# Kernel tuning notes

Measured on AMD Instinct MI355X. Metric: run time of the kernel, lower is better.

Reference implementation:

```python
import jax, jax.numpy as jnp
import numpy as np

INF = 1.0e10
EPS = 1e-12

def setup_inputs() -> dict:
    key = jax.random.key(0)
    k1, k2 = jax.random.split(key)
    B, N, A = 512, 16384, 64
    return {
        "residue_ca_pos": jax.random.normal(k1, (B, N, 3), dtype=jnp.float32) * 10.0,
        "residue_mask": jnp.ones((B, N), dtype=jnp.float32),
        "atom_pos": jax.random.normal(k2, (B, A, 3), dtype=jnp.float32) * 10.0,
        "atom_mask": jnp.ones((B, A), dtype=jnp.float32),
        "max_p": 1,
        "top_k": 4096,
    }

def reference(residue_ca_pos, residue_mask, atom_pos, atom_mask, max_p, top_k):
    # ligand centroid per batch: [B, 3]
    centroid = atom_pos.sum(-2) / atom_mask.sum(-1, keepdims=True)
    # distance from centroid to each residue Ca, invalid residues pushed to +inf
    diff = centroid[:, None, :] - residue_ca_pos            # [B, N, 3]
    dists = jnp.sqrt(jnp.sum(diff * diff, axis=-1) + EPS) + (1.0 - residue_mask) * INF
    # k smallest distances -> neighbor indices [B, top_k]
    _, nbr_indices = jax.lax.top_k(-dists, top_k)
    rows = jnp.arange(residue_mask.shape[0])[:, None]       # [B, 1]
    # scatter writes building the masks (faithful to torch scatter_ with constants)
    residue_spatial_mask = residue_mask.at[rows, nbr_indices].set(0.0)
    residue_spatial_mask_esm = (1.0 - residue_mask).at[rows, nbr_indices].set(32.0)
    return residue_spatial_mask, residue_spatial_mask_esm
```

## Files before the change

kernel.cpp:

```cpp
#include <hip/hip_runtime.h>

#pragma clang fp contract(off)

#define B_   512
#define N_   16384
#define A_   64
#define TPB  1024
#define CAP  2048
#define ITERS 4

__global__ __launch_bounds__(TPB) void fused_kernel(
    const float* __restrict__ pos,   const float* __restrict__ mask,
    const float* __restrict__ apos,  const float* __restrict__ amask,
    const int*   __restrict__ topk_ptr,
    float* __restrict__ out0, float* __restrict__ out1)
{
#pragma clang fp contract(off)
    __shared__ unsigned short dist16[N_];
    __shared__ unsigned       hist[2048];
    __shared__ unsigned       hist2[32];
    __shared__ unsigned       cand_bits[CAP];
    __shared__ unsigned short cand_idx[CAP];
    __shared__ float          s_atoms[A_ * 3 + A_];
    __shared__ float          s_c[3];
    __shared__ unsigned       s_B11, s_less11, s_P16, s_j, s_ncand, s_k;

    const int tid = threadIdx.x;
    const int b   = blockIdx.x;
    const float* __restrict__ p = pos  + (size_t)b * N_ * 3;
    const float* __restrict__ m = mask + (size_t)b * N_;

    hist[tid]        = 0u;
    hist[tid + 1024] = 0u;
    if (tid < 32) hist2[tid] = 0u;
    if (tid < 256)
        s_atoms[tid] = (tid < 192) ? apos[(size_t)b * 192 + tid]
                                   : amask[(size_t)b * 64 + (tid - 192)];
    if (tid == 0) {
        s_ncand = 0u;
        int kk = *topk_ptr;
        if (kk < 0)  kk = 0;
        if (kk > N_) kk = N_;
        s_k = (unsigned)kk;
    }
    __syncthreads();

    if (tid < 64) {
        float comp = 0.0f, ms = 0.0f;
        if (tid < 3) {
            comp = s_atoms[tid];
            for (int a = 1; a < A_; ++a) comp += s_atoms[a * 3 + tid];
        }
        if (tid == 3) {
            const float* am = s_atoms + 192;
            float r0 = am[0], r1 = am[1], r2 = am[2], r3 = am[3];
            float r4 = am[4], r5 = am[5], r6 = am[6], r7 = am[7];
            for (int i = 8; i < A_; i += 8) {
                r0 += am[i + 0]; r1 += am[i + 1]; r2 += am[i + 2]; r3 += am[i + 3];
                r4 += am[i + 4]; r5 += am[i + 5]; r6 += am[i + 6]; r7 += am[i + 7];
            }
            ms = ((r0 + r1) + (r2 + r3)) + ((r4 + r5) + (r6 + r7));
        }
        ms = __shfl(ms, 3, 64);
        if (tid < 3) s_c[tid] = comp / ms;
    }
    __syncthreads();

    const float cx = s_c[0], cy = s_c[1], cz = s_c[2];
    const unsigned k = s_k;

    unsigned rbits[ITERS * 4];
    float    rm[ITERS * 4];
#pragma unroll
    for (int it = 0; it < ITERS; ++it) {
        const int i0 = it * (TPB * 4) + tid * 4;
        const float4 pa = *(const float4*)(p + (size_t)i0 * 3);
        const float4 pb = *(const float4*)(p + (size_t)i0 * 3 + 4);
        const float4 pc = *(const float4*)(p + (size_t)i0 * 3 + 8);
        const float4 mv = *(const float4*)(m + i0);
        const float px[4] = {pa.x, pa.w, pb.z, pc.y};
        const float py[4] = {pa.y, pb.x, pb.w, pc.z};
        const float pz[4] = {pa.z, pb.y, pc.x, pc.w};
        const float mm[4] = {mv.x, mv.y, mv.z, mv.w};
        unsigned short loc[4];
#pragma unroll
        for (int j = 0; j < 4; ++j) {
            float dx = cx - px[j], dy = cy - py[j], dz = cz - pz[j];
            float dx2 = dx * dx, dy2 = dy * dy, dz2 = dz * dz;
            float s = (dx2 + dy2) + dz2;
            s = s + 1e-12f;
            float d = sqrtf(s);
            float im = (1.0f - mm[j]) * 1e10f;
            d = d + im;
            const unsigned bits = __float_as_uint(d);
            rbits[it * 4 + j] = bits;
            rm[it * 4 + j]    = mm[j];
            loc[j] = (unsigned short)(bits >> 16);
            atomicAdd(&hist[bits >> 21], 1u);
        }
        *(ushort4*)&dist16[i0] = make_ushort4(loc[0], loc[1], loc[2], loc[3]);
    }
    __syncthreads();

    if (k > 0) {
        if (tid < 64) {
            unsigned s = 0;
#pragma unroll
            for (int i = 0; i < 32; ++i) s += hist[tid * 32 + i];
            unsigned incl = s;
#pragma unroll
            for (int off = 1; off < 64; off <<= 1) {
                unsigned v = (unsigned)__shfl_up((int)incl, off, 64);
                if (tid >= off) incl += v;
            }
            unsigned long long bal = __ballot(incl >= k);
            const int g = __ffsll(bal) - 1;
            const unsigned cum1 = (unsigned)__shfl((int)(incl - s), g, 64);

            unsigned h2 = (tid < 32) ? hist[g * 32 + tid] : 0u;
            unsigned incl2 = h2;
#pragma unroll
            for (int off = 1; off < 64; off <<= 1) {
                unsigned v = (unsigned)__shfl_up((int)incl2, off, 64);
                if (tid >= off) incl2 += v;
            }
            unsigned long long bal2 = __ballot(tid < 32 && (cum1 + incl2 >= k));
            const int sb = __ffsll(bal2) - 1;
            const unsigned cum2 = cum1 + (unsigned)__shfl((int)(incl2 - h2), sb, 64);
            if (tid == 0) { s_B11 = (unsigned)(g * 32 + sb); s_less11 = cum2; }
        }
        __syncthreads();
        const unsigned B11 = s_B11;

#pragma unroll
        for (int x = 0; x < ITERS * 4; ++x) {
            const unsigned v = rbits[x] >> 16;
            if ((v >> 5) == B11) atomicAdd(&hist2[v & 31u], 1u);
        }
        __syncthreads();
        if (tid < 64) {
            unsigned h = (tid < 32) ? hist2[tid] : 0u;
            unsigned incl = h;
#pragma unroll
            for (int off = 1; off < 64; off <<= 1) {
                unsigned v = (unsigned)__shfl_up((int)incl, off, 64);
                if (tid >= off) incl += v;
            }
            const unsigned less11 = s_less11;
            unsigned long long bal = __ballot(tid < 32 && (less11 + incl >= k));
            const int sb = __ffsll(bal) - 1;
            const unsigned cumx = less11 + (unsigned)__shfl((int)(incl - h), sb, 64);
            if (tid == 0) { s_P16 = (B11 << 5) | (unsigned)sb; s_j = k - cumx; }
        }
        __syncthreads();
        const unsigned P16 = s_P16;
        const unsigned j   = s_j;

#pragma unroll
        for (int it = 0; it < ITERS; ++it) {
#pragma unroll
            for (int jj = 0; jj < 4; ++jj) {
                const unsigned bits = rbits[it * 4 + jj];
                if ((bits >> 16) == P16) {
                    const unsigned w = atomicAdd(&s_ncand, 1u);
                    if (w < CAP) {
                        cand_bits[w] = bits;
                        cand_idx[w]  = (unsigned short)(it * (TPB * 4) + tid * 4 + jj);
                    }
                }
            }
        }
        __syncthreads();

        const unsigned c = min(s_ncand, (unsigned)CAP);
        for (unsigned t = tid; t < c; t += TPB) {
            const unsigned bt = cand_bits[t];
            const unsigned it = cand_idx[t];
            unsigned rank = 0;
            for (unsigned u = 0; u < c; ++u) {
                const unsigned bu = cand_bits[u];
                rank += (bu < bt) || (bu == bt && (unsigned)cand_idx[u] < it);
            }
            if (rank < j) dist16[it] = 0;
        }
        __syncthreads();
    }

    const unsigned P16f = (k > 0) ? s_P16 : 0u;
#pragma unroll
    for (int it = 0; it < ITERS; ++it) {
        const int i0 = it * (TPB * 4) + tid * 4;
        const ushort4 dv = *(const ushort4*)&dist16[i0];
        const unsigned short dvs[4] = {dv.x, dv.y, dv.z, dv.w};
        float4 o0, o1;
        float* o0p = &o0.x; float* o1p = &o1.x;
#pragma unroll
        for (int jj = 0; jj < 4; ++jj) {
            const bool sel = (unsigned)dvs[jj] < P16f;
            const float mv = rm[it * 4 + jj];
            o0p[jj] = sel ? 0.0f  : mv;
            o1p[jj] = sel ? 32.0f : (1.0f - mv);
        }
        *(float4*)(out0 + (size_t)b * N_ + i0) = o0;
        *(float4*)(out1 + (size_t)b * N_ + i0) = o1;
    }
}

extern "C" void kernel_launch(void* const* d_in, const int* in_sizes, int n_in,
                              void* d_out, int out_size, void* d_ws, size_t ws_size,
                              hipStream_t stream) {
    const float* pos   = (const float*)d_in[0];
    const float* rmask = (const float*)d_in[1];
    const float* apos  = (const float*)d_in[2];
    const float* amask = (const float*)d_in[3];
    const int*   topk  = (const int*)d_in[5];

    float* out0 = (float*)d_out;
    float* out1 = out0 + (size_t)B_ * N_;

    fused_kernel<<<B_, TPB, 0, stream>>>(pos, rmask, apos, amask, topk, out0, out1);
}
```

Before: 210.2 us.

## Stream inputs via triple-buffered global_load_lds pipeline and drop LDS distance array

Replaces direct per-thread float4 global loads with a 3-deep ring of asynchronous global-to-LDS copies (global_load_lds) overlapped with distance computation, using explicit vmcnt waits and barriers per chunk. Removes the 16-bit distance array in LDS by encoding candidate slots into the register-held bits and storing selection flags per candidate. Output writes become scalar per-thread coalesced stores instead of float4. The change lowers LDS footprint for occupancy and overlaps load latency, but adds two barriers per chunk and narrower stores.

```diff
diff --git a/kernel.cpp b/kernel.cpp
--- a/kernel.cpp
+++ b/kernel.cpp
@@ -2,28 +2,38 @@
 
 #pragma clang fp contract(off)
 
-#define B_   512
-#define N_   16384
-#define A_   64
-#define TPB  1024
-#define CAP  2048
-#define ITERS 4
-
-__global__ __launch_bounds__(TPB) void fused_kernel(
+#define B_     512
+#define N_     16384
+#define A_     64
+#define TPB    1024
+#define CAP    2048
+#define NCHUNK 16
+#define NBUF   3
+
+#define AS1 __attribute__((address_space(1)))
+#define AS3 __attribute__((address_space(3)))
+
+__device__ __forceinline__ void gl2lds16(const float* g, float* l) {
+    __builtin_amdgcn_global_load_lds((const AS1 unsigned int*)g,
+                                     (AS3 unsigned int*)l, 16, 0, 0);
+}
+
+__global__ __launch_bounds__(TPB, 8) void fused_kernel(
     const float* __restrict__ pos,   const float* __restrict__ mask,
     const float* __restrict__ apos,  const float* __restrict__ amask,
     const int*   __restrict__ topk_ptr,
     float* __restrict__ out0, float* __restrict__ out1)
 {
 #pragma clang fp contract(off)
-    __shared__ unsigned short dist16[N_];
+    __shared__ __align__(16) float stage[NBUF][4096];
     __shared__ unsigned       hist[2048];
     __shared__ unsigned       hist2[32];
     __shared__ unsigned       cand_bits[CAP];
     __shared__ unsigned short cand_idx[CAP];
+    __shared__ unsigned char  sel_flags[CAP];
     __shared__ float          s_atoms[A_ * 3 + A_];
     __shared__ float          s_c[3];
-    __shared__ unsigned       s_B11, s_less11, s_P16, s_j, s_ncand, s_k;
+    __shared__ unsigned s_B11, s_less11, s_P16, s_j, s_ncand, s_k;
 
     const int tid = threadIdx.x;
     const int b   = blockIdx.x;
@@ -43,6 +53,15 @@
         if (kk > N_) kk = N_;
         s_k = (unsigned)kk;
     }
+
+    {
+        const float* g0 = (tid < 768) ? (p + tid * 4)            : (m + (tid - 768) * 4);
+        const float* g1 = (tid < 768) ? (p + 3072 + tid * 4)     : (m + 1024 + (tid - 768) * 4);
+        const float* g2 = (tid < 768) ? (p + 2 * 3072 + tid * 4) : (m + 2 * 1024 + (tid - 768) * 4);
+        gl2lds16(g0, &stage[0][tid * 4]);
+        gl2lds16(g1, &stage[1][tid * 4]);
+        gl2lds16(g2, &stage[2][tid * 4]);
+    }
     __syncthreads();
 
     if (tid < 64) {
@@ -69,36 +88,43 @@
     const float cx = s_c[0], cy = s_c[1], cz = s_c[2];
     const unsigned k = s_k;
 
-    unsigned rbits[ITERS * 4];
-    float    rm[ITERS * 4];
-#pragma unroll
-    for (int it = 0; it < ITERS; ++it) {
-        const int i0 = it * (TPB * 4) + tid * 4;
-        const float4 pa = *(const float4*)(p + (size_t)i0 * 3);
-        const float4 pb = *(const float4*)(p + (size_t)i0 * 3 + 4);
-        const float4 pc = *(const float4*)(p + (size_t)i0 * 3 + 8);
-        const float4 mv = *(const float4*)(m + i0);
-        const float px[4] = {pa.x, pa.w, pb.z, pc.y};
-        const float py[4] = {pa.y, pb.x, pb.w, pc.z};
-        const float pz[4] = {pa.z, pb.y, pc.x, pc.w};
-        const float mm[4] = {mv.x, mv.y, mv.z, mv.w};
-        unsigned short loc[4];
-#pragma unroll
-        for (int j = 0; j < 4; ++j) {
-            float dx = cx - px[j], dy = cy - py[j], dz = cz - pz[j];
-            float dx2 = dx * dx, dy2 = dy * dy, dz2 = dz * dz;
-            float s = (dx2 + dy2) + dz2;
-            s = s + 1e-12f;
-            float d = sqrtf(s);
-            float im = (1.0f - mm[j]) * 1e10f;
-            d = d + im;
-            const unsigned bits = __float_as_uint(d);
-            rbits[it * 4 + j] = bits;
-            rm[it * 4 + j]    = mm[j];
-            loc[j] = (unsigned short)(bits >> 16);
-            atomicAdd(&hist[bits >> 21], 1u);
-        }
-        *(ushort4*)&dist16[i0] = make_ushort4(loc[0], loc[1], loc[2], loc[3]);
+    unsigned rbits[NCHUNK];
+    float    rm[NCHUNK];
+
+#pragma unroll
+    for (int c = 0; c < NCHUNK; ++c) {
+        if (c <= NCHUNK - 3)      asm volatile("s_waitcnt vmcnt(2)" ::: "memory");
+        else if (c == NCHUNK - 2) asm volatile("s_waitcnt vmcnt(1)" ::: "memory");
+        else                      asm volatile("s_waitcnt vmcnt(0)" ::: "memory");
+        __builtin_amdgcn_s_barrier();
+        asm volatile("" ::: "memory");
+
+        const float* buf = stage[c % NBUF];
+        const float px = buf[3 * tid];
+        const float py = buf[3 * tid + 1];
+        const float pz = buf[3 * tid + 2];
+        const float mm = buf[3072 + tid];
+
+        float dx = cx - px, dy = cy - py, dz = cz - pz;
+        float dx2 = dx * dx, dy2 = dy * dy, dz2 = dz * dz;
+        float s = (dx2 + dy2) + dz2;
+        s = s + 1e-12f;
+        float d = sqrtf(s);
+        d = d + (1.0f - mm) * 1e10f;
+        const unsigned bits = __float_as_uint(d);
+        rbits[c] = bits;
+        rm[c]    = mm;
+        atomicAdd(&hist[bits >> 21], 1u);
+
+        asm volatile("s_waitcnt lgkmcnt(0)" ::: "memory");
+        __builtin_amdgcn_s_barrier();
+        asm volatile("" ::: "memory");
+        if (c + NBUF < NCHUNK) {
+            const float* g = (tid < 768)
+                ? (p + (size_t)(c + NBUF) * 3072 + tid * 4)
+                : (m + (size_t)(c + NBUF) * 1024 + (tid - 768) * 4);
+            gl2lds16(g, &stage[c % NBUF][tid * 4]);
+        }
     }
     __syncthreads();
 
@@ -133,7 +159,7 @@
         const unsigned B11 = s_B11;
 
 #pragma unroll
-        for (int x = 0; x < ITERS * 4; ++x) {
+        for (int x = 0; x < NCHUNK; ++x) {
             const unsigned v = rbits[x] >> 16;
             if ((v >> 5) == B11) atomicAdd(&hist2[v & 31u], 1u);
         }
@@ -157,52 +183,47 @@
         const unsigned j   = s_j;
 
 #pragma unroll
-        for (int it = 0; it < ITERS; ++it) {
-#pragma unroll
-            for (int jj = 0; jj < 4; ++jj) {
-                const unsigned bits = rbits[it * 4 + jj];
-                if ((bits >> 16) == P16) {
-                    const unsigned w = atomicAdd(&s_ncand, 1u);
-                    if (w < CAP) {
-                        cand_bits[w] = bits;
-                        cand_idx[w]  = (unsigned short)(it * (TPB * 4) + tid * 4 + jj);
-                    }
+        for (int c2 = 0; c2 < NCHUNK; ++c2) {
+            const unsigned bits = rbits[c2];
+            if ((bits >> 16) == P16) {
+                const unsigned w = atomicAdd(&s_ncand, 1u);
+                if (w < CAP) {
+                    cand_bits[w] = bits;
+                    cand_idx[w]  = (unsigned short)(c2 * 1024 + tid);
+                    rbits[c2] = 0xFFFF0000u | w;
                 }
             }
         }
         __syncthreads();
 
-        const unsigned c = min(s_ncand, (unsigned)CAP);
-        for (unsigned t = tid; t < c; t += TPB) {
+        const unsigned cnum = min(s_ncand, (unsigned)CAP);
+        for (unsigned t = tid; t < cnum; t += TPB) {
             const unsigned bt = cand_bits[t];
             const unsigned it = cand_idx[t];
             unsigned rank = 0;
-            for (unsigned u = 0; u < c; ++u) {
+            for (unsigned u = 0; u < cnum; ++u) {
                 const unsigned bu = cand_bits[u];
                 rank += (bu < bt) || (bu == bt && (unsigned)cand_idx[u] < it);
             }
-            if (rank < j) dist16[it] = 0;
+            sel_flags[t] = (rank < j) ? (unsigned char)1 : (unsigned char)0;
         }
         __syncthreads();
     }
 
     const unsigned P16f = (k > 0) ? s_P16 : 0u;
 #pragma unroll
-    for (int it = 0; it < ITERS; ++it) {
-        const int i0 = it * (TPB * 4) + tid * 4;
-        const ushort4 dv = *(const ushort4*)&dist16[i0];
-        const unsigned short dvs[4] = {dv.x, dv.y, dv.z, dv.w};
-        float4 o0, o1;
-        float* o0p = &o0.x; float* o1p = &o1.x;
-#pragma unroll
-        for (int jj = 0; jj < 4; ++jj) {
-            const bool sel = (unsigned)dvs[jj] < P16f;
-            const float mv = rm[it * 4 + jj];
-            o0p[jj] = sel ? 0.0f  : mv;
-            o1p[jj] = sel ? 32.0f : (1.0f - mv);
-        }
-        *(float4*)(out0 + (size_t)b * N_ + i0) = o0;
-        *(float4*)(out1 + (size_t)b * N_ + i0) = o1;
+    for (int c2 = 0; c2 < NCHUNK; ++c2) {
+        const unsigned v   = rbits[c2];
+        const unsigned v16 = v >> 16;
+        bool sel = false;
+        if (k > 0) {
+            sel = (v16 == 0xFFFFu) ? (sel_flags[v & (CAP - 1u)] != 0)
+                                   : (v16 < P16f);
+        }
+        const float mv = rm[c2];
+        const size_t o = (size_t)b * N_ + (size_t)c2 * 1024 + tid;
+        out0[o] = sel ? 0.0f  : mv;
+        out1[o] = sel ? 32.0f : (1.0f - mv);
     }
 }
 
```

After: 311.0 us. 1.48x slower.

## Aggregate histogram atomics per wave and drop shared dist16 array

Applied to the files above, without the earlier changes.

Replaces per-thread LDS atomics in both histogram passes with wave-level leader aggregation: each unique bucket in the wave gets one atomicAdd of its popcount. Candidate compaction now uses one atomic per wave plus ballot prefix offsets. The 32KB dist16 LDS buffer goes away; selection is resolved from the register-held bits plus a small per-candidate flag array. The centroid is broadcast by shuffles instead of through shared memory and a barrier. The aim is less LDS atomic contention and lower shared-memory use, at the cost of serial ballot loops when a wave's buckets are diverse.

```diff
diff --git a/kernel.cpp b/kernel.cpp
--- a/kernel.cpp
+++ b/kernel.cpp
@@ -7,7 +7,31 @@
 #define A_   64
 #define TPB  1024
 #define CAP  2048
-#define ITERS 4
+
+__device__ __forceinline__ void hist_add_wave(unsigned* hist, unsigned bucket) {
+    const int lane = threadIdx.x & 63;
+    unsigned long long rem = ~0ull;
+    while (rem) {
+        const int leader = __ffsll((long long)rem) - 1;
+        const unsigned vb = (unsigned)__shfl((int)bucket, leader, 64);
+        const unsigned long long same = __ballot(bucket == vb);
+        if (lane == leader) atomicAdd(&hist[vb], (unsigned)__popcll(same));
+        rem &= ~same;
+    }
+}
+
+__device__ __forceinline__ void hist_add_wave_pred(unsigned* hist,
+                                                   unsigned bucket, bool pred) {
+    const int lane = threadIdx.x & 63;
+    unsigned long long rem = __ballot(pred);
+    while (rem) {
+        const int leader = __ffsll((long long)rem) - 1;
+        const unsigned vb = (unsigned)__shfl((int)bucket, leader, 64);
+        const unsigned long long same = __ballot(pred && (bucket == vb));
+        if (lane == leader) atomicAdd(&hist[vb], (unsigned)__popcll(same));
+        rem &= ~same;
+    }
+}
 
 __global__ __launch_bounds__(TPB) void fused_kernel(
     const float* __restrict__ pos,   const float* __restrict__ mask,
@@ -16,16 +40,16 @@
     float* __restrict__ out0, float* __restrict__ out1)
 {
 #pragma clang fp contract(off)
-    __shared__ unsigned short dist16[N_];
     __shared__ unsigned       hist[2048];
     __shared__ unsigned       hist2[32];
     __shared__ unsigned       cand_bits[CAP];
     __shared__ unsigned short cand_idx[CAP];
+    __shared__ unsigned char  sel_flags[CAP];
     __shared__ float          s_atoms[A_ * 3 + A_];
-    __shared__ float          s_c[3];
-    __shared__ unsigned       s_B11, s_less11, s_P16, s_j, s_ncand, s_k;
+    __shared__ unsigned s_B11, s_less11, s_P16, s_j, s_ncand, s_k;
 
     const int tid = threadIdx.x;
+    const int l   = tid & 63;
     const int b   = blockIdx.x;
     const float* __restrict__ p = pos  + (size_t)b * N_ * 3;
     const float* __restrict__ m = mask + (size_t)b * N_;
@@ -45,13 +69,14 @@
     }
     __syncthreads();
 
-    if (tid < 64) {
+    float cx, cy, cz;
+    {
         float comp = 0.0f, ms = 0.0f;
-        if (tid < 3) {
-            comp = s_atoms[tid];
-            for (int a = 1; a < A_; ++a) comp += s_atoms[a * 3 + tid];
-        }
-        if (tid == 3) {
+        if (l < 3) {
+            comp = s_atoms[l];
+            for (int a = 1; a < A_; ++a) comp += s_atoms[a * 3 + l];
+        }
+        if (l == 3) {
             const float* am = s_atoms + 192;
             float r0 = am[0], r1 = am[1], r2 = am[2], r3 = am[3];
             float r4 = am[4], r5 = am[5], r6 = am[6], r7 = am[7];
@@ -62,18 +87,19 @@
             ms = ((r0 + r1) + (r2 + r3)) + ((r4 + r5) + (r6 + r7));
         }
         ms = __shfl(ms, 3, 64);
-        if (tid < 3) s_c[tid] = comp / ms;
-    }
-    __syncthreads();
-
-    const float cx = s_c[0], cy = s_c[1], cz = s_c[2];
+        const float cc = (l < 3) ? comp / ms : 0.0f;
+        cx = __shfl(cc, 0, 64);
+        cy = __shfl(cc, 1, 64);
+        cz = __shfl(cc, 2, 64);
+    }
+
     const unsigned k = s_k;
 
-    unsigned rbits[ITERS * 4];
-    float    rm[ITERS * 4];
-#pragma unroll
-    for (int it = 0; it < ITERS; ++it) {
-        const int i0 = it * (TPB * 4) + tid * 4;
+    unsigned rbits[16];
+    float    rmv[16];
+#pragma unroll
+    for (int it = 0; it < 4; ++it) {
+        const int i0 = it * 4096 + tid * 4;
         const float4 pa = *(const float4*)(p + (size_t)i0 * 3);
         const float4 pb = *(const float4*)(p + (size_t)i0 * 3 + 4);
         const float4 pc = *(const float4*)(p + (size_t)i0 * 3 + 8);
@@ -82,7 +108,6 @@
         const float py[4] = {pa.y, pb.x, pb.w, pc.z};
         const float pz[4] = {pa.z, pb.y, pc.x, pc.w};
         const float mm[4] = {mv.x, mv.y, mv.z, mv.w};
-        unsigned short loc[4];
 #pragma unroll
         for (int j = 0; j < 4; ++j) {
             float dx = cx - px[j], dy = cy - py[j], dz = cz - pz[j];
@@ -90,15 +115,12 @@
             float s = (dx2 + dy2) + dz2;
             s = s + 1e-12f;
             float d = sqrtf(s);
-            float im = (1.0f - mm[j]) * 1e10f;
-            d = d + im;
+            d = d + (1.0f - mm[j]) * 1e10f;
             const unsigned bits = __float_as_uint(d);
             rbits[it * 4 + j] = bits;
-            rm[it * 4 + j]    = mm[j];
-            loc[j] = (unsigned short)(bits >> 16);
-            atomicAdd(&hist[bits >> 21], 1u);
-        }
-        *(ushort4*)&dist16[i0] = make_ushort4(loc[0], loc[1], loc[2], loc[3]);
+            rmv[it * 4 + j]   = mm[j];
+            hist_add_wave(hist, bits >> 21);
+        }
     }
     __syncthreads();
 
@@ -133,9 +155,9 @@
         const unsigned B11 = s_B11;
 
 #pragma unroll
-        for (int x = 0; x < ITERS * 4; ++x) {
+        for (int x = 0; x < 16; ++x) {
             const unsigned v = rbits[x] >> 16;
-            if ((v >> 5) == B11) atomicAdd(&hist2[v & 31u], 1u);
+            hist_add_wave_pred(hist2, v & 31u, (v >> 5) == B11);
         }
         __syncthreads();
         if (tid < 64) {
@@ -157,49 +179,60 @@
         const unsigned j   = s_j;
 
 #pragma unroll
-        for (int it = 0; it < ITERS; ++it) {
-#pragma unroll
-            for (int jj = 0; jj < 4; ++jj) {
-                const unsigned bits = rbits[it * 4 + jj];
-                if ((bits >> 16) == P16) {
-                    const unsigned w = atomicAdd(&s_ncand, 1u);
-                    if (w < CAP) {
-                        cand_bits[w] = bits;
-                        cand_idx[w]  = (unsigned short)(it * (TPB * 4) + tid * 4 + jj);
-                    }
+        for (int x = 0; x < 16; ++x) {
+            const unsigned bits = rbits[x];
+            const bool pred = (bits >> 16) == P16;
+            const unsigned long long pm = __ballot(pred);
+            if (pred) {
+                const int leader = __ffsll((long long)pm) - 1;
+                unsigned base = 0;
+                if (l == leader)
+                    base = atomicAdd(&s_ncand, (unsigned)__popcll(pm));
+                base = (unsigned)__shfl((int)base, leader, 64);
+                const unsigned w = base
+                    + (unsigned)__popcll(pm & ((1ull << l) - 1ull));
+                if (w < CAP) {
+                    cand_bits[w] = bits;
+                    cand_idx[w]  = (unsigned short)((x >> 2) * 4096 + tid * 4
+                                                    + (x & 3));
+                    rbits[x] = 0xFFFF0000u | w;
                 }
             }
         }
         __syncthreads();
 
-        const unsigned c = min(s_ncand, (unsigned)CAP);
-        for (unsigned t = tid; t < c; t += TPB) {
+        const unsigned cnum = min(s_ncand, (unsigned)CAP);
+        for (unsigned t = tid; t < cnum; t += TPB) {
             const unsigned bt = cand_bits[t];
             const unsigned it = cand_idx[t];
             unsigned rank = 0;
-            for (unsigned u = 0; u < c; ++u) {
+            for (unsigned u = 0; u < cnum; ++u) {
                 const unsigned bu = cand_bits[u];
                 rank += (bu < bt) || (bu == bt && (unsigned)cand_idx[u] < it);
             }
-            if (rank < j) dist16[it] = 0;
+            sel_flags[t] = (rank < j) ? (unsigned char)1 : (unsigned char)0;
         }
         __syncthreads();
     }
 
     const unsigned P16f = (k > 0) ? s_P16 : 0u;
 #pragma unroll
-    for (int it = 0; it < ITERS; ++it) {
-        const int i0 = it * (TPB * 4) + tid * 4;
-        const ushort4 dv = *(const ushort4*)&dist16[i0];
-        const unsigned short dvs[4] = {dv.x, dv.y, dv.z, dv.w};
+    for (int it = 0; it < 4; ++it) {
+        const int i0 = it * 4096 + tid * 4;
         float4 o0, o1;
         float* o0p = &o0.x; float* o1p = &o1.x;
 #pragma unroll
         for (int jj = 0; jj < 4; ++jj) {
-            const bool sel = (unsigned)dvs[jj] < P16f;
-            const float mv = rm[it * 4 + jj];
-            o0p[jj] = sel ? 0.0f  : mv;
-            o1p[jj] = sel ? 32.0f : (1.0f - mv);
+            const unsigned v   = rbits[it * 4 + jj];
+            const unsigned v16 = v >> 16;
+            bool sel = false;
+            if (k > 0) {
+                sel = (v16 == 0xFFFFu) ? (sel_flags[v & (CAP - 1u)] != 0)
+                                       : (v16 < P16f);
+            }
+            const float mvv = rmv[it * 4 + jj];
+            o0p[jj] = sel ? 0.0f  : mvv;
+            o1p[jj] = sel ? 32.0f : (1.0f - mvv);
         }
         *(float4*)(out0 + (size_t)b * N_ + i0) = o0;
         *(float4*)(out1 + (size_t)b * N_ + i0) = o1;
```

Result: slower. 246.1 us (+17.1%).
